# Kernel tuning notes

Hardware: AMD Instinct MI355X
Metric: run time of the kernel (lower is better)

## Reference

```python
import jax, jax.numpy as jnp
import numpy as np

B, LENGTH = 4, 65494
FILTS = 256        # sinc out channels == attention seq len == d_model (BN constraint)
KERNEL = 1025      # first_conv=1024 -> forced odd
D_MODEL = 256
N_HEADS = 8
D_FF = 1024
E_LAYERS = 4
C_OUT = 2
IN_SIZE = 21490
SR = 16000


def _to_mel(hz):
    return 2595 * np.log10(1 + hz / 700)


def _to_hz(mel):
    return 700 * (10 ** (mel / 2595) - 1)


def make_sinc_filters():
    out_ch = FILTS + 1
    f = (SR // 2) * np.linspace(0, 1, 257)  # NFFT=512 -> 257 bins
    fmel = _to_mel(f)
    mels = np.linspace(fmel.min(), fmel.max(), out_ch + 2)
    freq = _to_hz(mels)[:out_ch]
    hsupp = np.arange(-(KERNEL - 1) / 2, (KERNEL - 1) / 2 + 1)
    ham = np.hamming(KERNEL)
    bp = np.zeros((FILTS, KERNEL), dtype=np.float32)
    for i in range(FILTS):
        fmin, fmax = freq[i], freq[i + 1]
        h_hi = 2 * fmax / SR * np.sinc(2 * fmax * hsupp / SR)
        h_lo = 2 * fmin / SR * np.sinc(2 * fmin * hsupp / SR)
        bp[i] = (ham * (h_hi - h_lo)).astype(np.float32)
    return jnp.asarray(bp).reshape(FILTS, 1, KERNEL)


def layernorm(x, g, b, eps=1e-5):
    m = x.mean(-1, keepdims=True)
    v = x.var(-1, keepdims=True)
    return (x - m) / jnp.sqrt(v + eps) * g + b


def batchnorm(x, g, b, eps=1e-5):
    # training-mode BatchNorm1d over [B, C, T]: stats over (0, 2)
    m = x.mean((0, 2), keepdims=True)
    v = x.var((0, 2), keepdims=True)
    return (x - m) / jnp.sqrt(v + eps) * g[None, :, None] + b[None, :, None]


def positional(n):
    pos = jnp.arange(n, dtype=jnp.float32)[:, None]
    div = jnp.exp(jnp.arange(0, D_MODEL, 2, dtype=jnp.float32) * (-np.log(10000.0) / D_MODEL))
    pe = jnp.zeros((n, D_MODEL), jnp.float32)
    pe = pe.at[:, 0::2].set(jnp.sin(pos * div)).at[:, 1::2].set(jnp.cos(pos * div))
    return pe


def _forward(x, filters, bn1_g, bn1_b, emb_w, emb_b, embbn_g, embbn_b,
             wq, bq, wk, bk, wv, bv, wo, bo, c1w, c1b, c2w, c2b,
             ln1g, ln1b, ln2g, ln2b, lnfg, lnfb, projw, projb):
    Bb = x.shape[0]
    # SincConv: [B,1,L] -> [B, FILTS, L-K+1]
    h = jax.lax.conv_general_dilated(x[:, None, :], filters, (1,), 'VALID',
                                     dimension_numbers=('NCH', 'OIH', 'NCH'))
    h = jnp.abs(h)
    T = h.shape[-1] // 3
    h = h[..., :T * 3].reshape(Bb, FILTS, T, 3).max(-1)  # max_pool1d(k=3)
    h = jax.nn.selu(batchnorm(h, bn1_g, bn1_b))          # [B, FILTS, 21490]
    # LinearEmbedding: Linear(21490 -> d_model) + BN + ReLU + pos emb
    e = jnp.einsum('bct,dt->bcd', h, emb_w) + emb_b      # [B, FILTS, D_MODEL]
    e = jax.nn.relu(batchnorm(e, embbn_g, embbn_b))
    z = e + positional(e.shape[1])[None]
    hd = D_MODEL // N_HEADS
    scale = 1.0 / np.sqrt(hd)
    for l in range(E_LAYERS):
        q = (z @ wq[l].T + bq[l]).reshape(Bb, FILTS, N_HEADS, hd)
        k = (z @ wk[l].T + bk[l]).reshape(Bb, FILTS, N_HEADS, hd)
        v = (z @ wv[l].T + bv[l]).reshape(Bb, FILTS, N_HEADS, hd)
        scores = jnp.einsum('blhe,bshe->bhls', q, k) * scale  # mask_flag=False
        attn = jax.nn.softmax(scores, axis=-1)
        o = jnp.einsum('bhls,bshd->blhd', attn, v).reshape(Bb, FILTS, D_MODEL)
        o = o @ wo[l].T + bo[l]
        z = layernorm(z + o, ln1g[l], ln1b[l])
        y = jax.nn.gelu(jnp.einsum('bld,fd->blf', z, c1w[l]) + c1b[l], approximate=False)
        y = jnp.einsum('blf,df->bld', y, c2w[l]) + c2b[l]
        z = layernorm(z + y, ln2g[l], ln2b[l])
    z = layernorm(z, lnfg, lnfb)
    pooled = z.mean(axis=1)
    return pooled @ projw.T + projb  # [B, C_OUT]


def setup_inputs() -> dict:
    key = jax.random.key(0)
    ks = jax.random.split(key, 16)
    rn = lambda k, s, sc=0.02: jax.random.normal(k, s, jnp.float32) * sc
    d = {}
    d['x'] = jax.random.normal(ks[0], (B, LENGTH), jnp.float32)
    d['filters'] = make_sinc_filters()
    d['bn1_g'] = jnp.ones((FILTS,), jnp.float32)
    d['bn1_b'] = jnp.zeros((FILTS,), jnp.float32)
    d['emb_w'] = rn(ks[1], (D_MODEL, IN_SIZE))
    d['emb_b'] = jnp.zeros((D_MODEL,), jnp.float32)
    d['embbn_g'] = jnp.ones((D_MODEL,), jnp.float32)
    d['embbn_b'] = jnp.zeros((D_MODEL,), jnp.float32)
    d['wq'] = rn(ks[2], (E_LAYERS, D_MODEL, D_MODEL))
    d['bq'] = jnp.zeros((E_LAYERS, D_MODEL), jnp.float32)
    d['wk'] = rn(ks[3], (E_LAYERS, D_MODEL, D_MODEL))
    d['bk'] = jnp.zeros((E_LAYERS, D_MODEL), jnp.float32)
    d['wv'] = rn(ks[4], (E_LAYERS, D_MODEL, D_MODEL))
    d['bv'] = jnp.zeros((E_LAYERS, D_MODEL), jnp.float32)
    d['wo'] = rn(ks[5], (E_LAYERS, D_MODEL, D_MODEL))
    d['bo'] = jnp.zeros((E_LAYERS, D_MODEL), jnp.float32)
    d['c1w'] = rn(ks[6], (E_LAYERS, D_FF, D_MODEL))
    d['c1b'] = jnp.zeros((E_LAYERS, D_FF), jnp.float32)
    d['c2w'] = rn(ks[7], (E_LAYERS, D_MODEL, D_FF))
    d['c2b'] = jnp.zeros((E_LAYERS, D_MODEL), jnp.float32)
    d['ln1g'] = jnp.ones((E_LAYERS, D_MODEL), jnp.float32)
    d['ln1b'] = jnp.zeros((E_LAYERS, D_MODEL), jnp.float32)
    d['ln2g'] = jnp.ones((E_LAYERS, D_MODEL), jnp.float32)
    d['ln2b'] = jnp.zeros((E_LAYERS, D_MODEL), jnp.float32)
    d['lnfg'] = jnp.ones((D_MODEL,), jnp.float32)
    d['lnfb'] = jnp.zeros((D_MODEL,), jnp.float32)
    d['projw'] = rn(ks[8], (C_OUT, D_MODEL))
    d['projb'] = jnp.zeros((C_OUT,), jnp.float32)
    return d


def reference(x, filters, bn1_g, bn1_b, emb_w, emb_b, embbn_g, embbn_b,
              wq, bq, wk, bk, wv, bv, wo, bo, c1w, c1b, c2w, c2b,
              ln1g, ln1b, ln2g, ln2b, lnfg, lnfb, projw, projb):
    return _forward(x, filters, bn1_g, bn1_b, emb_w, emb_b, embbn_g, embbn_b,
                    wq, bq, wk, bk, wv, bv, wo, bo, c1w, c1b, c2w, c2b,
                    ln1g, ln1b, ln2g, ln2b, lnfg, lnfb, projw, projb)
```

## Files before the change

kernel.cpp:

```cpp
#include <hip/hip_runtime.h>
#include <math.h>

#define L_IN 65494
#define T_POOL 21490
#define TPP 21496
#define KF 1025
#define RS 1144
#define NCH 141
#define KEMB 21490
#define KEMBP 21504
#define NKC 1344
#define FTILE 33280
#define LWSZ 786432

typedef short s16x4 __attribute__((ext_vector_type(4)));
typedef _Float16 f16x8 __attribute__((ext_vector_type(8)));
typedef float f32x4 __attribute__((ext_vector_type(4)));
typedef float f32x16 __attribute__((ext_vector_type(16)));

__device__ inline float selu_f(float x) {
    float e = expf(fminf(x, 0.f));
    float neg = 1.6732632423543772f * (e - 1.f);
    return 1.0507009873554805f * (x > 0.f ? x : neg);
}

__device__ inline float gelu_f(float x) {
    return 0.5f * x * (1.f + erff(x * 0.7071067811865476f));
}

__device__ inline float dot4(float4 a, float4 b) {
    return fmaf(a.x, b.x, fmaf(a.y, b.y, fmaf(a.z, b.z, a.w * b.w)));
}

__device__ inline float sel4(float a0, float a1, float a2, float a3, int i) {
    float r = a0;
    r = (i == 1) ? a1 : r;
    r = (i == 2) ? a2 : r;
    r = (i == 3) ? a3 : r;
    return r;
}

__device__ inline short f2h_bits(float v) {
    _Float16 h = (_Float16)v;
    return *(short*)&h;
}

__device__ inline void f16split2(float v, _Float16& h, _Float16& l) {
    h = (_Float16)v;
    l = (_Float16)(v - (float)h);
}

__global__ __launch_bounds__(512)
void pack_all_kernel(const float* __restrict__ filt, const float* __restrict__ emb_w,
                     const float* __restrict__ wo, const float* __restrict__ wq,
                     const float* __restrict__ wk, const float* __restrict__ wv,
                     const float* __restrict__ c1w, const float* __restrict__ c2w,
                     short* __restrict__ fpH, short* __restrict__ wpH,
                     short* __restrict__ lw) {
    int bx = blockIdx.x;
    int t = threadIdx.x, lane = t >> 3, e = t & 7;
    if (bx < 520) {
        int ft = bx / 65, kc = bx % 65;
        int f = ft * 32 + (lane & 31);
        int tap = kc * 16 + (lane >> 5) * 8 + e;
        float v = (tap < KF) ? filt[f * KF + tap] : 0.f;
        fpH[bx * 512 + t] = f2h_bits(v);
    } else if (bx < 520 + 8 * NKC) {
        int blk = bx - 520;
        int ft = blk / NKC, kc = blk % NKC;
        int row = ft * 32 + (lane & 31);
        int tap = kc * 16 + (lane >> 5) * 8 + e;
        float v = (tap < KEMB) ? emb_w[(long)row * KEMB + tap] : 0.f;
        wpH[(long)blk * 512 + t] = f2h_bits(v);
    } else {
        int b = bx - 520 - 8 * NKC;
        int layer = b / 1536, r = b % 1536;
        const float* src;
        int K, t2;
        long dst;
        if (r < 512) {
            int mat = r >> 7; t2 = r & 127;
            const float* m0 = (mat == 0 ? wo : mat == 1 ? wq : mat == 2 ? wk : wv);
            src = m0 + (long)layer * 65536; K = 256;
            dst = (long)layer * LWSZ + (long)mat * 65536 + (long)t2 * 512;
        } else if (r < 1024) {
            t2 = r - 512;
            src = c1w + (long)layer * 262144; K = 256;
            dst = (long)layer * LWSZ + 262144 + (long)t2 * 512;
        } else {
            t2 = r - 1024;
            src = c2w + (long)layer * 262144; K = 1024;
            dst = (long)layer * LWSZ + 524288 + (long)t2 * 512;
        }
        int KB = K >> 5;
        int nt = t2 / KB, kb = t2 % KB;
        int n = nt * 16 + (lane & 15);
        int k = kb * 32 + ((lane >> 4) & 3) * 8 + e;
        lw[dst + t] = f2h_bits(src[(long)n * K + k]);
    }
}

__device__ inline f32x4 mfma_nt(const _Float16* __restrict__ Xh, const _Float16* __restrict__ Xl,
                                int xstride, const short* __restrict__ wp_nt, int KB, int lane) {
    f32x4 acc = {0.f, 0.f, 0.f, 0.f};
    const int row = (lane & 15) & 3;
    const int ko0 = ((lane >> 4) & 3) * 8;
    const short* bp = wp_nt + lane * 8;
    const _Float16* xh = Xh + row * xstride + ko0;
    const _Float16* xl = Xl + row * xstride + ko0;
#pragma unroll 4
    for (int kb = 0; kb < KB; kb++) {
        f16x8 bf = *(const f16x8*)(bp + kb * 512);
        f16x8 ah = *(const f16x8*)(xh + kb * 32);
        f16x8 al = *(const f16x8*)(xl + kb * 32);
        acc = __builtin_amdgcn_mfma_f32_16x16x32_f16(al, bf, acc, 0, 0, 0);
        acc = __builtin_amdgcn_mfma_f32_16x16x32_f16(ah, bf, acc, 0, 0, 0);
    }
    return acc;
}

union ConvLDS {
    short xh[8][RS];
    float ebuf[96][129];
};

__global__ __launch_bounds__(256, 3)
void conv_mfma_kernel(const float* __restrict__ x, const short* __restrict__ fpH,
                      _Float16* __restrict__ h) {
    __shared__ ConvLDS u;
    const int tid = threadIdx.x;
    const int pb = blockIdx.x;
    const int b = blockIdx.y;
    const int t0 = pb * 96;
    const float* xb = x + (long)b * L_IN;

    if (pb < 671) {
        for (int idx = tid; idx < 8 * NCH; idx += 256) {
            int s = idx / NCH, j = idx - s * NCH;
            int gi = t0 + s + j * 8;
            f16x8 hv;
#pragma unroll
            for (int e = 0; e < 8; e++) hv[e] = (_Float16)xb[gi + e];
            *(f16x8*)&u.xh[s][j * 8] = hv;
        }
    } else {
        for (int idx = tid; idx < 8 * NCH; idx += 256) {
            int s = idx / NCH, j = idx - s * NCH;
            int gi = t0 + s + j * 8;
            f16x8 hv;
#pragma unroll
            for (int e = 0; e < 8; e++) {
                float v = (gi + e < L_IN) ? xb[gi + e] : 0.f;
                hv[e] = (_Float16)v;
            }
            *(f16x8*)&u.xh[s][j * 8] = hv;
        }
    }
    __syncthreads();

    const int lane = tid & 63;
    const int wid = tid >> 6;
    const int l31 = lane & 31;
    const int hi = lane >> 5;
    const int f0w = wid * 64;

    const short* aH = &u.xh[l31 & 7][8 * (l31 >> 3) + 8 * hi];
    const short* bp0 = fpH + (long)(wid * 2) * FTILE + lane * 8;
    const short* bp1 = bp0 + FTILE;

    f32x16 a00 = {0}, a01 = {0}, a10 = {0}, a11 = {0}, a20 = {0}, a21 = {0};

#pragma unroll 1
    for (int kc = 0; kc < 65; kc++) {
        const int ko = kc * 16;
        const int kf = kc * 512;
        f16x8 ah0 = *(const f16x8*)(aH + ko);
        f16x8 ah1 = *(const f16x8*)(aH + ko + 32);
        f16x8 ah2 = *(const f16x8*)(aH + ko + 64);
        f16x8 bh0 = *(const f16x8*)(bp0 + kf);
        f16x8 bh1 = *(const f16x8*)(bp1 + kf);
        a00 = __builtin_amdgcn_mfma_f32_32x32x16_f16(ah0, bh0, a00, 0, 0, 0);
        a01 = __builtin_amdgcn_mfma_f32_32x32x16_f16(ah0, bh1, a01, 0, 0, 0);
        a10 = __builtin_amdgcn_mfma_f32_32x32x16_f16(ah1, bh0, a10, 0, 0, 0);
        a11 = __builtin_amdgcn_mfma_f32_32x32x16_f16(ah1, bh1, a11, 0, 0, 0);
        a20 = __builtin_amdgcn_mfma_f32_32x32x16_f16(ah2, bh0, a20, 0, 0, 0);
        a21 = __builtin_amdgcn_mfma_f32_32x32x16_f16(ah2, bh1, a21, 0, 0, 0);
    }

    __syncthreads();
    const int t3l = tid & 31;
    const int t3 = pb * 32 + t3l;

#pragma unroll
    for (int half = 0; half < 2; half++) {
        if ((wid >> 1) == half) {
            int fcb = f0w - half * 128;
#define WRF(ACC, MT, NT)                                                   \
            {                                                              \
                int fc = fcb + NT * 32 + l31;                              \
                _Pragma("unroll")                                          \
                for (int r = 0; r < 16; r++) {                             \
                    int pos = MT * 32 + (r & 3) + 8 * (r >> 2) + 4 * hi;   \
                    u.ebuf[pos][fc] = fabsf(ACC[r]);                       \
                }                                                          \
            }
            WRF(a00, 0, 0) WRF(a01, 0, 1)
            WRF(a10, 1, 0) WRF(a11, 1, 1)
            WRF(a20, 2, 0) WRF(a21, 2, 1)
#undef WRF
        }
        __syncthreads();
        if (t3 < T_POOL) {
            for (int ff = tid >> 5; ff < 128; ff += 8) {
                float v = fmaxf(fmaxf(u.ebuf[3 * t3l][ff], u.ebuf[3 * t3l + 1][ff]),
                                u.ebuf[3 * t3l + 2][ff]);
                h[((long)(b * 256 + half * 128 + ff)) * TPP + t3] = (_Float16)v;
            }
        }
        __syncthreads();
    }
}

__global__ __launch_bounds__(256)
void bn_part_kernel(const _Float16* __restrict__ xin, float* __restrict__ p1,
                    float* __restrict__ p2) {
    __shared__ float sm[8];
    int c = blockIdx.x, s = blockIdx.y, tid = threadIdx.x;
    int t0 = s * 2687, t1 = min(T_POOL, t0 + 2687);
    float s1 = 0.f, s2 = 0.f;
    for (int b = 0; b < 4; b++) {
        const _Float16* p = xin + (long)b * 256 * TPP + (long)c * TPP;
        for (int t = t0 + tid; t < t1; t += 256) {
            float v = (float)p[t];
            s1 += v;
            s2 = fmaf(v, v, s2);
        }
    }
    for (int off = 32; off > 0; off >>= 1) { s1 += __shfl_down(s1, off); s2 += __shfl_down(s2, off); }
    int lane = tid & 63, wv = tid >> 6;
    if (lane == 0) { sm[wv] = s1; sm[4 + wv] = s2; }
    __syncthreads();
    if (tid == 0) {
        p1[c * 8 + s] = sm[0] + sm[1] + sm[2] + sm[3];
        p2[c * 8 + s] = sm[4] + sm[5] + sm[6] + sm[7];
    }
}

__global__ __launch_bounds__(256)
void bn_fin_kernel(const float* __restrict__ p1, const float* __restrict__ p2,
                   const float* __restrict__ g, const float* __restrict__ bb,
                   float* __restrict__ sc, float* __restrict__ sh) {
    int c = threadIdx.x;
    float S1 = 0.f, S2 = 0.f;
#pragma unroll
    for (int s = 0; s < 8; s++) { S1 += p1[c * 8 + s]; S2 += p2[c * 8 + s]; }
    float n = 4.f * (float)T_POOL;
    float mean = S1 / n;
    float var = S2 / n - mean * mean;
    float rstd = rsqrtf(var + 1e-5f);
    float gc = g[c], bc = bb[c];
    sc[c] = rstd * gc;
    sh[c] = bc - mean * rstd * gc;
}

__global__ __launch_bounds__(256, 2)
void embed_mfma_kernel(const _Float16* __restrict__ H, const short* __restrict__ Wh,
                       const float* __restrict__ sc, const float* __restrict__ sh,
                       float* __restrict__ P, int kPerZ) {
    __shared__ short Ah[128][36];
    const int tid = threadIdx.x;
    const int rowBase = blockIdx.x * 128;
    const int colBase = blockIdx.y * 128;
    const int z = blockIdx.z;
    const int kz = z * kPerZ;
    const int iters = kPerZ >> 5;

    const int trow = tid >> 1, th = (tid & 1) * 16;
    const int arow = rowBase + trow;
    const float asc = sc[arow & 255], ash_ = sh[arow & 255];
    const _Float16* Ap = H + (long)arow * TPP;

    const int lane = tid & 63, wid = tid >> 6;
    const int l31 = lane & 31, hi = lane >> 5;
    const int wm = wid >> 1, wn = wid & 1;

    const short* bhp[2];
#pragma unroll
    for (int nt = 0; nt < 2; nt++) {
        int ft = (colBase >> 5) + wn * 2 + nt;
        bhp[nt] = Wh + (long)ft * NKC * 512 + lane * 8;
    }

    f32x16 acc[2][2] = {{{0}, {0}}, {{0}, {0}}};

    for (int it = 0; it < iters; it++) {
        const int k0 = kz + it * 32;
        __syncthreads();
        float av[16];
        if (k0 + 32 <= KEMB) {
            const f16x8* p8 = (const f16x8*)(Ap + k0 + th);
            f16x8 v0 = p8[0], v1 = p8[1];
#pragma unroll
            for (int e = 0; e < 8; e++) { av[e] = (float)v0[e]; av[8 + e] = (float)v1[e]; }
        } else {
#pragma unroll
            for (int e = 0; e < 16; e++) {
                int k = k0 + th + e;
                av[e] = (k < KEMB) ? (float)Ap[k] : 0.f;
            }
        }
#pragma unroll
        for (int q = 0; q < 4; q++) {
            s16x4 h4;
#pragma unroll
            for (int e = 0; e < 4; e++) {
                float v = selu_f(fmaf(av[q * 4 + e], asc, ash_));
                h4[e] = f2h_bits(v);
            }
            *(s16x4*)&Ah[trow][th + q * 4] = h4;
        }
        __syncthreads();

#pragma unroll
        for (int ks = 0; ks < 2; ks++) {
            const int kloc = ks * 16 + hi * 8;
            const long kcg = (long)((k0 >> 4) + ks) * 512;
            f16x8 ah[2], bh[2];
#pragma unroll
            for (int mt = 0; mt < 2; mt++) {
                const int r = wm * 64 + mt * 32 + l31;
                const short* ph = &Ah[r][kloc];
                union { f16x8 v; unsigned long long q[2]; } uh;
                uh.q[0] = *(const unsigned long long*)(ph);
                uh.q[1] = *(const unsigned long long*)(ph + 4);
                ah[mt] = uh.v;
            }
#pragma unroll
            for (int nt = 0; nt < 2; nt++)
                bh[nt] = *(const f16x8*)(bhp[nt] + kcg);
#pragma unroll
            for (int mt = 0; mt < 2; mt++)
#pragma unroll
                for (int nt = 0; nt < 2; nt++)
                    acc[mt][nt] = __builtin_amdgcn_mfma_f32_32x32x16_f16(ah[mt], bh[nt], acc[mt][nt], 0, 0, 0);
        }
    }

    float* Pz = P + (long)z * 262144;
#pragma unroll
    for (int mt = 0; mt < 2; mt++)
#pragma unroll
        for (int nt = 0; nt < 2; nt++) {
            int col = colBase + wn * 64 + nt * 32 + l31;
#pragma unroll
            for (int r = 0; r < 16; r++) {
                int row = rowBase + wm * 64 + mt * 32 + (r & 3) + 8 * (r >> 2) + 4 * hi;
                Pz[(long)row * 256 + col] = acc[mt][nt][r];
            }
        }
}

__global__ __launch_bounds__(256)
void embed_combine_kernel(const float* __restrict__ P, const float* __restrict__ eb,
                          float* __restrict__ e, float* __restrict__ ebnp, int nsplit) {
    __shared__ float sm[8];
    const int bid = blockIdx.x, tid = threadIdx.x;
    const int idx = bid * 256 + tid;
    float s = 0.f;
    for (int z = 0; z < nsplit; z++) s += P[(long)z * 262144 + idx];
    float v = s + eb[tid];
    e[idx] = v;
    float s1 = v, s2 = v * v;
    for (int off = 32; off > 0; off >>= 1) { s1 += __shfl_down(s1, off); s2 += __shfl_down(s2, off); }
    int lane = tid & 63, wv = tid >> 6;
    if (lane == 0) { sm[wv] = s1; sm[4 + wv] = s2; }
    __syncthreads();
    if (tid == 0) {
        ebnp[bid * 2] = sm[0] + sm[1] + sm[2] + sm[3];
        ebnp[bid * 2 + 1] = sm[4] + sm[5] + sm[6] + sm[7];
    }
}

__global__ __launch_bounds__(512)
void qkv_init_kernel(const float* __restrict__ e, const float* __restrict__ ebnp,
                     const float* __restrict__ bng, const float* __restrict__ bnb,
                     const short* __restrict__ lw0,
                     const float* __restrict__ bq0, const float* __restrict__ bk0,
                     const float* __restrict__ bv0,
                     float* __restrict__ z, float* __restrict__ qo,
                     float* __restrict__ ko, float* __restrict__ vo) {
    __shared__ _Float16 zsh[4][256], zsl[4][256];
    __shared__ float scs[4], shs[4];
    const int t = threadIdx.x;
    const int w = t >> 6, lane = t & 63;
    const long rowg0 = (long)blockIdx.x * 4;

    if (t < 4) {
        int c = (int)((rowg0 + t) & 255);
        float S1 = 0.f, S2 = 0.f;
#pragma unroll
        for (int b2 = 0; b2 < 4; b2++) {
            S1 += ebnp[(b2 * 256 + c) * 2];
            S2 += ebnp[(b2 * 256 + c) * 2 + 1];
        }
        float mean = S1 * (1.f / 1024.f);
        float var = S2 * (1.f / 1024.f) - mean * mean;
        float rstd = rsqrtf(var + 1e-5f);
        float gc = bng[c];
        scs[t] = rstd * gc;
        shs[t] = bnb[c] - mean * rstd * gc;
    }
    __syncthreads();

    for (int idx = t; idx < 1024; idx += 512) {
        int i = idx >> 8, dd = idx & 255;
        int c = (int)((rowg0 + i) & 255);
        float v = fmaf(e[(rowg0 + i) * 256 + dd], scs[i], shs[i]);
        v = fmaxf(v, 0.f);
        int i2 = dd >> 1;
        float ang = (float)c * expf(-0.03597789207803195f * (float)(2 * i2));
        float pe = (dd & 1) ? cosf(ang) : sinf(ang);
        float zz = v + pe;
        z[(rowg0 + i) * 256 + dd] = zz;
        _Float16 hh, ll;
        f16split2(zz, hh, ll);
        zsh[i][dd] = hh; zsl[i][dd] = ll;
    }
    __syncthreads();

#pragma unroll
    for (int mat = 0; mat < 3; mat++) {
        const short* wp = lw0 + 65536 * (1 + mat);
        const float* bb = (mat == 0 ? bq0 : mat == 1 ? bk0 : bv0);
        float* op = (mat == 0 ? qo : mat == 1 ? ko : vo);
        for (int nt = w; nt < 16; nt += 8) {
            f32x4 acc = mfma_nt(&zsh[0][0], &zsl[0][0], 256, wp + nt * 8 * 512, 8, lane);
            if (lane < 16) {
                int col = nt * 16 + lane;
                float bv2 = bb[col];
#pragma unroll
                for (int r = 0; r < 4; r++)
                    op[(rowg0 + r) * 256 + col] = acc[r] + bv2;
            }
        }
    }
}

__device__ inline void ln_reduce4(const float (*buf)[256], float (*mr)[2], int t) {
    int wid = t >> 6, lane = t & 63;
    if (wid < 4) {
        float4 v = *(const float4*)&buf[wid][lane * 4];
        float s = v.x + v.y + v.z + v.w;
        float q = v.x * v.x + v.y * v.y + v.z * v.z + v.w * v.w;
#pragma unroll
        for (int off = 32; off > 0; off >>= 1) {
            s += __shfl_xor(s, off);
            q += __shfl_xor(q, off);
        }
        if (lane == 0) {
            float mean = s * (1.f / 256.f);
            float var = q * (1.f / 256.f) - mean * mean;
            mr[wid][0] = mean;
            mr[wid][1] = rsqrtf(var + 1e-5f);
        }
    }
}

template <int LAST>
__global__ __launch_bounds__(1024)
void layer_kernel(const float* __restrict__ zin, const float* __restrict__ qin,
                  const float* __restrict__ kin, const float* __restrict__ vin,
                  const short* __restrict__ lw_l, const short* __restrict__ lw_n,
                  const float* __restrict__ bo_l,
                  const float* __restrict__ c1b_l, const float* __restrict__ c2b_l,
                  const float* __restrict__ ln1g_l, const float* __restrict__ ln1b_l,
                  const float* __restrict__ ln2g_l, const float* __restrict__ ln2b_l,
                  const float* __restrict__ bq_n, const float* __restrict__ bk_n,
                  const float* __restrict__ bv_n,
                  const float* __restrict__ lnfg, const float* __restrict__ lnfb,
                  float* __restrict__ zout, float* __restrict__ qo,
                  float* __restrict__ ko, float* __restrict__ vo,
                  float* __restrict__ lnf_out) {
    __shared__ float zs[4][256];
    __shared__ float qb[4][256];
    __shared__ float sscore[4][8][256];
    __shared__ _Float16 zsh[4][256], zsl[4][256];
    __shared__ _Float16 yh[4][1024], yl[4][1024];
    __shared__ float mr[4][2];

    const int t = threadIdx.x;
    const int w = t >> 6, lane = t & 63;
    const long rowg0 = (long)blockIdx.x * 4;
    const int b = blockIdx.x >> 6;

    const int f = t & 255;
    const int kq = t >> 8;

    {
        int r = t >> 8, dd = t & 255;
        zs[r][dd] = zin[(rowg0 + r) * 256 + dd];
        qb[r][dd] = qin[(rowg0 + r) * 256 + dd];
    }
    __syncthreads();

    {
        const float scale = 0.17677669529663687f;
        const int jq = lane >> 3, li = lane & 7, d4 = li * 4;
        const int hh = w >> 1, jh = w & 1;
        const float* kb = kin + (long)b * 65536 + hh * 32 + d4;
        float4 q0 = *(const float4*)&qb[0][hh * 32 + d4];
        float4 q1 = *(const float4*)&qb[1][hh * 32 + d4];
        float4 q2 = *(const float4*)&qb[2][hh * 32 + d4];
        float4 q3 = *(const float4*)&qb[3][hh * 32 + d4];
        for (int jb = 0; jb < 16; jb++) {
            int j = jh * 128 + jb * 8 + jq;
            float4 kv = *(const float4*)(kb + (long)j * 256);
            float a0 = dot4(kv, q0), a1 = dot4(kv, q1);
            float a2 = dot4(kv, q2), a3 = dot4(kv, q3);
#pragma unroll
            for (int off = 1; off < 8; off <<= 1) {
                a0 += __shfl_xor(a0, off); a1 += __shfl_xor(a1, off);
                a2 += __shfl_xor(a2, off); a3 += __shfl_xor(a3, off);
            }
            if (li < 4) sscore[li][hh][j] = sel4(a0, a1, a2, a3, li) * scale;
        }
    }
    __syncthreads();

    {
#pragma unroll
        for (int p = 0; p < 2; p++) {
            int pair = w * 2 + p;
            int i = pair >> 3, hh = pair & 7;
            float* row = sscore[i][hh];
            float v0 = row[lane], v1 = row[lane + 64];
            float v2 = row[lane + 128], v3 = row[lane + 192];
            float m = fmaxf(fmaxf(v0, v1), fmaxf(v2, v3));
#pragma unroll
            for (int off = 32; off > 0; off >>= 1) m = fmaxf(m, __shfl_xor(m, off));
            float e0 = expf(v0 - m), e1 = expf(v1 - m);
            float e2 = expf(v2 - m), e3 = expf(v3 - m);
            float su = e0 + e1 + e2 + e3;
#pragma unroll
            for (int off = 32; off > 0; off >>= 1) su += __shfl_xor(su, off);
            float inv = 1.f / su;
            row[lane] = e0 * inv; row[lane + 64] = e1 * inv;
            row[lane + 128] = e2 * inv; row[lane + 192] = e3 * inv;
        }
    }
    __syncthreads();

    {
        int row = kq;
        int hh = f >> 5;
        const float* vcol = vin + (long)b * 65536 + f;
        const float* p0 = sscore[row][hh];
        float a0 = 0.f;
#pragma unroll 4
        for (int j4 = 0; j4 < 64; j4++) {
            float4 pv0 = *(const float4*)(p0 + j4 * 4);
            float v0 = vcol[(long)(j4 * 4 + 0) * 256];
            float v1 = vcol[(long)(j4 * 4 + 1) * 256];
            float v2 = vcol[(long)(j4 * 4 + 2) * 256];
            float v3 = vcol[(long)(j4 * 4 + 3) * 256];
            a0 = fmaf(pv0.x, v0, a0); a0 = fmaf(pv0.y, v1, a0);
            a0 = fmaf(pv0.z, v2, a0); a0 = fmaf(pv0.w, v3, a0);
        }
        _Float16 hh2, ll;
        f16split2(a0, hh2, ll);
        zsh[row][f] = hh2; zsl[row][f] = ll;
    }
    __syncthreads();

    {
        int nt = w;
        f32x4 acc = mfma_nt(&zsh[0][0], &zsl[0][0], 256, lw_l + nt * 8 * 512, 8, lane);
        if (lane < 16) {
            int col = nt * 16 + lane;
            float bb = bo_l[col];
#pragma unroll
            for (int r = 0; r < 4; r++)
                qb[r][col] = acc[r] + bb + zs[r][col];
        }
    }
    __syncthreads();
    ln_reduce4(qb, mr, t);
    __syncthreads();
    {
        int r = kq;
        float z1 = (qb[r][f] - mr[r][0]) * mr[r][1] * ln1g_l[f] + ln1b_l[f];
        zs[r][f] = z1;
        _Float16 hh2, ll;
        f16split2(z1, hh2, ll);
        zsh[r][f] = hh2; zsl[r][f] = ll;
    }
    __syncthreads();

    {
        const short* wp = lw_l + 262144;
        for (int nt = w; nt < 64; nt += 16) {
            f32x4 acc = mfma_nt(&zsh[0][0], &zsl[0][0], 256, wp + nt * 8 * 512, 8, lane);
            if (lane < 16) {
                int col = nt * 16 + lane;
                float cb = c1b_l[col];
#pragma unroll
                for (int r = 0; r < 4; r++) {
                    float g = gelu_f(acc[r] + cb);
                    _Float16 hh2, ll;
                    f16split2(g, hh2, ll);
                    yh[r][col] = hh2; yl[r][col] = ll;
                }
            }
        }
    }
    __syncthreads();

    {
        const short* wp = lw_l + 524288;
        int nt = w;
        f32x4 acc = mfma_nt(&yh[0][0], &yl[0][0], 1024, wp + nt * 32 * 512, 32, lane);
        if (lane < 16) {
            int col = nt * 16 + lane;
            float cb = c2b_l[col];
#pragma unroll
            for (int r = 0; r < 4; r++)
                qb[r][col] = acc[r] + cb + zs[r][col];
        }
    }
    __syncthreads();
    ln_reduce4(qb, mr, t);
    __syncthreads();
    {
        int r = kq;
        float z2 = (qb[r][f] - mr[r][0]) * mr[r][1] * ln2g_l[f] + ln2b_l[f];
        zs[r][f] = z2;
        zout[(rowg0 + r) * 256 + f] = z2;
        _Float16 hh2, ll;
        f16split2(z2, hh2, ll);
        zsh[r][f] = hh2; zsl[r][f] = ll;
    }
    __syncthreads();

    if (!LAST) {
#pragma unroll
        for (int mat = 0; mat < 3; mat++) {
            const short* wp = lw_n + 65536 * (1 + mat);
            const float* bb = (mat == 0 ? bq_n : mat == 1 ? bk_n : bv_n);
            float* op = (mat == 0 ? qo : mat == 1 ? ko : vo);
            int nt = w;
            f32x4 acc = mfma_nt(&zsh[0][0], &zsl[0][0], 256, wp + nt * 8 * 512, 8, lane);
            if (lane < 16) {
                int col = nt * 16 + lane;
                float bv2 = bb[col];
#pragma unroll
                for (int r = 0; r < 4; r++)
                    op[(rowg0 + r) * 256 + col] = acc[r] + bv2;
            }
        }
    } else {
        ln_reduce4(zs, mr, t);
        __syncthreads();
        {
            int r = kq;
            lnf_out[(rowg0 + r) * 256 + f] =
                (zs[r][f] - mr[r][0]) * mr[r][1] * lnfg[f] + lnfb[f];
        }
    }
}

__global__ __launch_bounds__(256)
void final_kernel(const float* __restrict__ zf, const float* __restrict__ pw,
                  const float* __restrict__ pb, float* __restrict__ out) {
    __shared__ float sm[8];
    int b = blockIdx.x, d = threadIdx.x;
    float s = 0.f;
    for (int c = 0; c < 256; c++) s += zf[((long)(b * 256 + c)) * 256 + d];
    float pooled = s * (1.f / 256.f);
    float c0 = pooled * pw[d], c1 = pooled * pw[256 + d];
    for (int off = 32; off > 0; off >>= 1) { c0 += __shfl_down(c0, off); c1 += __shfl_down(c1, off); }
    int lane = d & 63, wv = d >> 6;
    if (lane == 0) { sm[wv] = c0; sm[4 + wv] = c1; }
    __syncthreads();
    if (d == 0) {
        out[b * 2 + 0] = sm[0] + sm[1] + sm[2] + sm[3] + pb[0];
        out[b * 2 + 1] = sm[4] + sm[5] + sm[6] + sm[7] + pb[1];
    }
}

extern "C" void kernel_launch(void* const* d_in, const int* in_sizes, int n_in,
                              void* d_out, int out_size, void* d_ws, size_t ws_size,
                              hipStream_t stream) {
    const float* x       = (const float*)d_in[0];
    const float* filters = (const float*)d_in[1];
    const float* bn1_g   = (const float*)d_in[2];
    const float* bn1_b   = (const float*)d_in[3];
    const float* emb_w   = (const float*)d_in[4];
    const float* emb_b   = (const float*)d_in[5];
    const float* embbn_g = (const float*)d_in[6];
    const float* embbn_b = (const float*)d_in[7];
    const float* wq      = (const float*)d_in[8];
    const float* bq      = (const float*)d_in[9];
    const float* wk      = (const float*)d_in[10];
    const float* bk      = (const float*)d_in[11];
    const float* wv      = (const float*)d_in[12];
    const float* bv      = (const float*)d_in[13];
    const float* wo      = (const float*)d_in[14];
    const float* bo      = (const float*)d_in[15];
    const float* c1w     = (const float*)d_in[16];
    const float* c1b     = (const float*)d_in[17];
    const float* c2w     = (const float*)d_in[18];
    const float* c2b     = (const float*)d_in[19];
    const float* ln1g    = (const float*)d_in[20];
    const float* ln1b    = (const float*)d_in[21];
    const float* ln2g    = (const float*)d_in[22];
    const float* ln2b    = (const float*)d_in[23];
    const float* lnfg    = (const float*)d_in[24];
    const float* lnfb    = (const float*)d_in[25];
    const float* projw   = (const float*)d_in[26];
    const float* projb   = (const float*)d_in[27];

    const long hF = 11005952L;
    const long wpackF = 2752512L;
    const long lwF = 1572864L;
    const long fixedF = hF + 6656 + wpackF + lwF + 9L * 262144;
    long wsFloats = (long)(ws_size / 4);
    long Z = 32;
    while (Z > 8 && fixedF + Z * 262144L > wsFloats) Z >>= 1;
    const int kPerZ = KEMBP / (int)Z;

    float* ws = (float*)d_ws;
    _Float16* h16 = (_Float16*)ws;
    float* bn1_sc = ws + hF;
    float* bn1_sh = bn1_sc + 256;
    float* ebnp   = bn1_sh + 256;
    float* bnp1   = ebnp + 2048;
    float* bnp2   = bnp1 + 2048;
    float* part   = bnp2 + 2048;
    float* wsp    = part + Z * 262144L;
    short* wpH    = (short*)wsp;
    float* e      = wsp + wpackF;
    float* z      = e + 262144;
    float* qA     = z + 262144;
    float* kA     = qA + 262144;
    float* vA     = kA + 262144;
    float* qB     = vA + 262144;
    float* kB     = qB + 262144;
    float* vB     = kB + 262144;
    float* t1     = vB + 262144;
    short* lw     = (short*)(t1 + 262144);

    short* fpH = (short*)part;

    pack_all_kernel<<<520 + 8 * NKC + 6144, 512, 0, stream>>>(
        filters, emb_w, wo, wq, wk, wv, c1w, c2w, fpH, wpH, lw);
    conv_mfma_kernel<<<dim3(672, 4), 256, 0, stream>>>(x, fpH, h16);
    bn_part_kernel<<<dim3(256, 8), 256, 0, stream>>>(h16, bnp1, bnp2);
    bn_fin_kernel<<<1, 256, 0, stream>>>(bnp1, bnp2, bn1_g, bn1_b, bn1_sc, bn1_sh);
    embed_mfma_kernel<<<dim3(8, 2, (int)Z), 256, 0, stream>>>(h16, wpH,
                                                              bn1_sc, bn1_sh, part, kPerZ);
    embed_combine_kernel<<<1024, 256, 0, stream>>>(part, emb_b, e, ebnp, (int)Z);
    qkv_init_kernel<<<256, 512, 0, stream>>>(e, ebnp, embbn_g, embbn_b, lw,
                                             bq, bk, bv, z, qA, kA, vA);

    float* qs[2][3] = {{qA, kA, vA}, {qB, kB, vB}};
    for (int l = 0; l < 4; l++) {
        float** in = qs[l & 1];
        float** ou = qs[(l + 1) & 1];
        const short* lw_l = lw + (long)l * LWSZ;
        const short* lw_n = lw + (long)((l + 1) & 3) * LWSZ;
        const float* bo_l = bo + l * 256;
        const float* c1b_l = c1b + l * 1024;
        const float* c2b_l = c2b + l * 256;
        const float* l1g = ln1g + l * 256; const float* l1b = ln1b + l * 256;
        const float* l2g = ln2g + l * 256; const float* l2b = ln2b + l * 256;
        if (l < 3) {
            const float* bq_n = bq + (l + 1) * 256;
            const float* bk_n = bk + (l + 1) * 256;
            const float* bv_n = bv + (l + 1) * 256;
            layer_kernel<0><<<256, 1024, 0, stream>>>(z, in[0], in[1], in[2],
                lw_l, lw_n, bo_l, c1b_l, c2b_l, l1g, l1b, l2g, l2b,
                bq_n, bk_n, bv_n, lnfg, lnfb,
                z, ou[0], ou[1], ou[2], t1);
        } else {
            layer_kernel<1><<<256, 1024, 0, stream>>>(z, in[0], in[1], in[2],
                lw_l, lw_n, bo_l, c1b_l, c2b_l, l1g, l1b, l2g, l2b,
                bq, bk, bv, lnfg, lnfb,
                z, ou[0], ou[1], ou[2], t1);
        }
    }

    final_kernel<<<4, 256, 0, stream>>>(t1, projw, projb, (float*)d_out);
}
```

Baseline: 450.5 us.

## Split sinc conv filters across grid z to halve per-block accumulators

The sinc convolution kernel now launches twice as many blocks, each covering half the filters (128 instead of 256). Each wave keeps three 32x32 accumulators instead of six, and the LDS epilogue buffer shrinks to 32 columns, drained in four passes. This cuts register and LDS pressure to raise occupancy and expose more parallelism. The cost is that every block re-stages the input window into LDS, so input staging is done twice, and the epilogue needs more barriers.

Result: slower. 463.4 us (+2.9%).

```diff
diff --git a/kernel.cpp b/kernel.cpp
--- a/kernel.cpp
+++ b/kernel.cpp
@@ -121,16 +121,17 @@
 
 union ConvLDS {
     short xh[8][RS];
-    float ebuf[96][129];
+    float ebuf[96][33];
 };
 
-__global__ __launch_bounds__(256, 3)
+__global__ __launch_bounds__(256)
 void conv_mfma_kernel(const float* __restrict__ x, const short* __restrict__ fpH,
                       _Float16* __restrict__ h) {
     __shared__ ConvLDS u;
     const int tid = threadIdx.x;
     const int pb = blockIdx.x;
     const int b = blockIdx.y;
+    const int fg = blockIdx.z;
     const int t0 = pb * 96;
     const float* xb = x + (long)b * L_IN;
 
@@ -162,13 +163,11 @@
     const int wid = tid >> 6;
     const int l31 = lane & 31;
     const int hi = lane >> 5;
-    const int f0w = wid * 64;
 
     const short* aH = &u.xh[l31 & 7][8 * (l31 >> 3) + 8 * hi];
-    const short* bp0 = fpH + (long)(wid * 2) * FTILE + lane * 8;
-    const short* bp1 = bp0 + FTILE;
-
-    f32x16 a00 = {0}, a01 = {0}, a10 = {0}, a11 = {0}, a20 = {0}, a21 = {0};
+    const short* bp = fpH + (long)(fg * 4 + wid) * FTILE + lane * 8;
+
+    f32x16 a0 = {0}, a1 = {0}, a2 = {0};
 
 #pragma unroll 1
     for (int kc = 0; kc < 65; kc++) {
@@ -177,48 +176,40 @@
         f16x8 ah0 = *(const f16x8*)(aH + ko);
         f16x8 ah1 = *(const f16x8*)(aH + ko + 32);
         f16x8 ah2 = *(const f16x8*)(aH + ko + 64);
-        f16x8 bh0 = *(const f16x8*)(bp0 + kf);
-        f16x8 bh1 = *(const f16x8*)(bp1 + kf);
-        a00 = __builtin_amdgcn_mfma_f32_32x32x16_f16(ah0, bh0, a00, 0, 0, 0);
-        a01 = __builtin_amdgcn_mfma_f32_32x32x16_f16(ah0, bh1, a01, 0, 0, 0);
-        a10 = __builtin_amdgcn_mfma_f32_32x32x16_f16(ah1, bh0, a10, 0, 0, 0);
-        a11 = __builtin_amdgcn_mfma_f32_32x32x16_f16(ah1, bh1, a11, 0, 0, 0);
-        a20 = __builtin_amdgcn_mfma_f32_32x32x16_f16(ah2, bh0, a20, 0, 0, 0);
-        a21 = __builtin_amdgcn_mfma_f32_32x32x16_f16(ah2, bh1, a21, 0, 0, 0);
+        f16x8 bh = *(const f16x8*)(bp + kf);
+        a0 = __builtin_amdgcn_mfma_f32_32x32x16_f16(ah0, bh, a0, 0, 0, 0);
+        a1 = __builtin_amdgcn_mfma_f32_32x32x16_f16(ah1, bh, a1, 0, 0, 0);
+        a2 = __builtin_amdgcn_mfma_f32_32x32x16_f16(ah2, bh, a2, 0, 0, 0);
     }
 
     __syncthreads();
     const int t3l = tid & 31;
     const int t3 = pb * 32 + t3l;
-
-#pragma unroll
-    for (int half = 0; half < 2; half++) {
-        if ((wid >> 1) == half) {
-            int fcb = f0w - half * 128;
-#define WRF(ACC, MT, NT)                                                   \
-            {                                                              \
-                int fc = fcb + NT * 32 + l31;                              \
-                _Pragma("unroll")                                          \
-                for (int r = 0; r < 16; r++) {                             \
-                    int pos = MT * 32 + (r & 3) + 8 * (r >> 2) + 4 * hi;   \
-                    u.ebuf[pos][fc] = fabsf(ACC[r]);                       \
-                }                                                          \
-            }
-            WRF(a00, 0, 0) WRF(a01, 0, 1)
-            WRF(a10, 1, 0) WRF(a11, 1, 1)
-            WRF(a20, 2, 0) WRF(a21, 2, 1)
-#undef WRF
-        }
+    const int c0 = tid >> 5;
+
+#define WRF1(ACC, MT)                                                      \
+    {                                                                      \
+        _Pragma("unroll")                                                  \
+        for (int r = 0; r < 16; r++) {                                     \
+            int pos = MT * 32 + (r & 3) + 8 * (r >> 2) + 4 * hi;           \
+            u.ebuf[pos][l31] = fabsf(ACC[r]);                              \
+        }                                                                  \
+    }
+#pragma unroll 1
+    for (int fb = 0; fb < 4; fb++) {
+        if (wid == fb) { WRF1(a0, 0) WRF1(a1, 1) WRF1(a2, 2) }
         __syncthreads();
         if (t3 < T_POOL) {
-            for (int ff = tid >> 5; ff < 128; ff += 8) {
-                float v = fmaxf(fmaxf(u.ebuf[3 * t3l][ff], u.ebuf[3 * t3l + 1][ff]),
-                                u.ebuf[3 * t3l + 2][ff]);
-                h[((long)(b * 256 + half * 128 + ff)) * TPP + t3] = (_Float16)v;
+#pragma unroll
+            for (int cc = c0; cc < 32; cc += 8) {
+                float v = fmaxf(fmaxf(u.ebuf[3 * t3l][cc], u.ebuf[3 * t3l + 1][cc]),
+                                u.ebuf[3 * t3l + 2][cc]);
+                h[((long)(b * 256 + fg * 128 + fb * 32 + cc)) * TPP + t3] = (_Float16)v;
             }
         }
         __syncthreads();
     }
+#undef WRF1
 }
 
 __global__ __launch_bounds__(256)
@@ -753,7 +744,7 @@
 
     pack_all_kernel<<<520 + 8 * NKC + 6144, 512, 0, stream>>>(
         filters, emb_w, wo, wq, wk, wv, c1w, c2w, fpH, wpH, lw);
-    conv_mfma_kernel<<<dim3(672, 4), 256, 0, stream>>>(x, fpH, h16);
+    conv_mfma_kernel<<<dim3(672, 4, 2), 256, 0, stream>>>(x, fpH, h16);
     bn_part_kernel<<<dim3(256, 8), 256, 0, stream>>>(h16, bnp1, bnp2);
     bn_fin_kernel<<<1, 256, 0, stream>>>(bnp1, bnp2, bn1_g, bn1_b, bn1_sc, bn1_sh);
     embed_mfma_kernel<<<dim3(8, 2, (int)Z), 256, 0, stream>>>(h16, wpH,
```
